# Performance work log

Hardware: AMD Instinct MI355X
Metric: run time of the kernel (lower is better)

The kernel has to match this reference:

```python
import jax, jax.numpy as jnp
import numpy as np

B = 262144
PI = float(np.pi)

# Panda DH constants (theta is the joint variable): columns (d, a, alpha)
_D  = np.array([0.333, 0.0, 0.316, 0.0, 0.384, 0.0, 0.107], dtype=np.float32)
_A  = np.array([0.0, 0.0, 0.0, 0.0825, -0.0825, 0.0, 0.088], dtype=np.float32)
_AL = np.array([0.0, -PI/2, PI/2, PI/2, -PI/2, PI/2, PI/2], dtype=np.float32)


def setup_inputs() -> dict:
    key = jax.random.key(0)
    k1, k2 = jax.random.split(key)
    joints = jax.random.normal(k1, (B, 7), dtype=jnp.float32)
    poses = jax.random.normal(k2, (B, 6), dtype=jnp.float32)
    return {"joints": joints, "poses": poses}


def _fk_pose(joints):
    # joints: [B,7] -> [B,6] (xyz position + XYZ Euler angles)
    d = jnp.asarray(_D)
    a = jnp.asarray(_A)
    al = jnp.asarray(_AL)
    ct, st = jnp.cos(joints), jnp.sin(joints)          # [B,7]
    cal, sal = jnp.cos(al), jnp.sin(al)                # [7]
    zeros = jnp.zeros_like(ct)
    ones = jnp.ones_like(ct)
    # A matrices, batched over B and joint index: [B,7,4,4]
    r0 = jnp.stack([ct, -st * cal, st * sal, a * ct], axis=-1)
    r1 = jnp.stack([st, ct * cal, -ct * sal, a * st], axis=-1)
    r2 = jnp.stack([zeros, sal * ones, cal * ones, d * ones], axis=-1)
    r3 = jnp.stack([zeros, zeros, zeros, ones], axis=-1)
    A = jnp.stack([r0, r1, r2, r3], axis=-2)           # [B,7,4,4]
    # Chain of 4x4 transforms: T = A0 @ A1 @ ... @ A6
    T = A[:, 0]
    for i in range(1, 7):
        T = jnp.einsum('bij,bjk->bik', T, A[:, i])
    pos = T[:, :3, 3]                                   # [B,3]
    R = T[:, :3, :3]
    # matrix_to_euler_angles(R, 'XYZ'):
    #   [atan2(-R12, R22), asin(R02), atan2(-R01, R00)]
    rpy = jnp.stack([
        jnp.arctan2(-R[:, 1, 2], R[:, 2, 2]),
        jnp.arcsin(R[:, 0, 2]),
        jnp.arctan2(-R[:, 0, 1], R[:, 0, 0]),
    ], axis=-1)                                         # [B,3]
    return jnp.concatenate([pos, rpy], axis=-1)         # [B,6]


def reference(joints, poses):
    joints_fk = _fk_pose(joints)
    return jnp.mean((joints_fk - poses) ** 2)
```

## Files before the change

kernel.cpp:

```cpp
#include <hip/hip_runtime.h>


#define FK_B 262144

__device__ __forceinline__ void dh_step(float R[3][3], float p[3],
                                        float ct, float st,
                                        float d, float a,
                                        float cal, float sal) {
    const float c0x = ct,        c0y = st,        c0z = 0.0f;
    const float c1x = -st * cal, c1y = ct * cal,  c1z = sal;
    const float c2x = st * sal,  c2y = -ct * sal, c2z = cal;
    const float px = a * ct, py = a * st, pz = d;

    float nR[3][3], np[3];
#pragma unroll
    for (int r = 0; r < 3; ++r) {
        nR[r][0] = R[r][0] * c0x + R[r][1] * c0y + R[r][2] * c0z;
        nR[r][1] = R[r][0] * c1x + R[r][1] * c1y + R[r][2] * c1z;
        nR[r][2] = R[r][0] * c2x + R[r][1] * c2y + R[r][2] * c2z;
        np[r]    = R[r][0] * px  + R[r][1] * py  + R[r][2] * pz + p[r];
    }
#pragma unroll
    for (int r = 0; r < 3; ++r) {
        R[r][0] = nR[r][0]; R[r][1] = nR[r][1]; R[r][2] = nR[r][2];
        p[r] = np[r];
    }
}

__global__ __launch_bounds__(256) void fk_loss_kernel(
    const float* __restrict__ joints,
    const float* __restrict__ poses,
    float* __restrict__ out)
{
    const int i = blockIdx.x * blockDim.x + threadIdx.x;

    float q[7];
#pragma unroll
    for (int k = 0; k < 7; ++k) q[k] = joints[i * 7 + k];

    float s[7], c[7];
#pragma unroll
    for (int k = 0; k < 7; ++k) sincosf(q[k], &s[k], &c[k]);

    float R[3][3] = {{c[0], -s[0], 0.0f},
                     {s[0],  c[0], 0.0f},
                     {0.0f,  0.0f, 1.0f}};
    float p[3] = {0.0f, 0.0f, 0.333f};

    dh_step(R, p, c[1], s[1], 0.0f,   0.0f,    0.0f, -1.0f);
    dh_step(R, p, c[2], s[2], 0.316f, 0.0f,    0.0f,  1.0f);
    dh_step(R, p, c[3], s[3], 0.0f,   0.0825f, 0.0f,  1.0f);
    dh_step(R, p, c[4], s[4], 0.384f,-0.0825f, 0.0f, -1.0f);
    dh_step(R, p, c[5], s[5], 0.0f,   0.0f,    0.0f,  1.0f);
    dh_step(R, p, c[6], s[6], 0.107f, 0.088f,  0.0f,  1.0f);

    float fk[6];
    fk[0] = p[0]; fk[1] = p[1]; fk[2] = p[2];
    fk[3] = atan2f(-R[1][2], R[2][2]);
    float r02 = fminf(1.0f, fmaxf(-1.0f, R[0][2]));
    fk[4] = asinf(r02);
    fk[5] = atan2f(-R[0][1], R[0][0]);

    float err = 0.0f;
#pragma unroll
    for (int k = 0; k < 6; ++k) {
        float dlt = fk[k] - poses[i * 6 + k];
        err += dlt * dlt;
    }

#pragma unroll
    for (int off = 32; off > 0; off >>= 1)
        err += __shfl_down(err, off, 64);

    __shared__ float wsum[4];
    const int lane = threadIdx.x & 63;
    const int wid  = threadIdx.x >> 6;
    if (lane == 0) wsum[wid] = err;
    __syncthreads();
    if (threadIdx.x == 0) {
        float v = wsum[0] + wsum[1] + wsum[2] + wsum[3];
        atomicAdd(out, v * (1.0f / (FK_B * 6.0f)));
    }
}

extern "C" void kernel_launch(void* const* d_in, const int* in_sizes, int n_in,
                              void* d_out, int out_size, void* d_ws, size_t ws_size,
                              hipStream_t stream) {
    const float* joints = (const float*)d_in[0];
    const float* poses  = (const float*)d_in[1];
    float* out = (float*)d_out;

    hipMemsetAsync(out, 0, sizeof(float), stream);

    fk_loss_kernel<<<FK_B / 256, 256, 0, stream>>>(joints, poses, out);
}
```

Measured before the change: 76.67 us.

## Use fast intrinsic sin/cos and replace atomic reduction with two-pass partials

```diff
diff --git a/kernel.cpp b/kernel.cpp
--- a/kernel.cpp
+++ b/kernel.cpp
@@ -2,6 +2,7 @@
 
 
 #define FK_B 262144
+#define NBLK (FK_B / 256)
 
 __device__ __forceinline__ void dh_step(float R[3][3], float p[3],
                                         float ct, float st,
@@ -30,7 +31,7 @@
 __global__ __launch_bounds__(256) void fk_loss_kernel(
     const float* __restrict__ joints,
     const float* __restrict__ poses,
-    float* __restrict__ out)
+    float* __restrict__ partials)
 {
     const int i = blockIdx.x * blockDim.x + threadIdx.x;
 
@@ -40,7 +41,10 @@
 
     float s[7], c[7];
 #pragma unroll
-    for (int k = 0; k < 7; ++k) sincosf(q[k], &s[k], &c[k]);
+    for (int k = 0; k < 7; ++k) {
+        s[k] = __sinf(q[k]);
+        c[k] = __cosf(q[k]);
+    }
 
     float R[3][3] = {{c[0], -s[0], 0.0f},
                      {s[0],  c[0], 0.0f},
@@ -77,10 +81,31 @@
     const int wid  = threadIdx.x >> 6;
     if (lane == 0) wsum[wid] = err;
     __syncthreads();
-    if (threadIdx.x == 0) {
-        float v = wsum[0] + wsum[1] + wsum[2] + wsum[3];
-        atomicAdd(out, v * (1.0f / (FK_B * 6.0f)));
-    }
+    if (threadIdx.x == 0)
+        partials[blockIdx.x] = wsum[0] + wsum[1] + wsum[2] + wsum[3];
+}
+
+__global__ __launch_bounds__(256) void fk_reduce_kernel(
+    const float* __restrict__ partials,
+    float* __restrict__ out)
+{
+    const int t = threadIdx.x;
+    float v = 0.0f;
+#pragma unroll
+    for (int k = 0; k < NBLK / 256; ++k)
+        v += partials[t + k * 256];
+
+#pragma unroll
+    for (int off = 32; off > 0; off >>= 1)
+        v += __shfl_down(v, off, 64);
+
+    __shared__ float wsum[4];
+    const int lane = t & 63;
+    const int wid  = t >> 6;
+    if (lane == 0) wsum[wid] = v;
+    __syncthreads();
+    if (t == 0)
+        out[0] = (wsum[0] + wsum[1] + wsum[2] + wsum[3]) * (1.0f / (FK_B * 6.0f));
 }
 
 extern "C" void kernel_launch(void* const* d_in, const int* in_sizes, int n_in,
@@ -88,9 +113,9 @@
                               hipStream_t stream) {
     const float* joints = (const float*)d_in[0];
     const float* poses  = (const float*)d_in[1];
-    float* out = (float*)d_out;
+    float* out      = (float*)d_out;
+    float* partials = (float*)d_ws;
 
-    hipMemsetAsync(out, 0, sizeof(float), stream);
-
-    fk_loss_kernel<<<FK_B / 256, 256, 0, stream>>>(joints, poses, out);
+    fk_loss_kernel<<<NBLK, 256, 0, stream>>>(joints, poses, partials);
+    fk_reduce_kernel<<<1, 256, 0, stream>>>(partials, out);
 }
```

After: 66.70 us. 13.0% less time.
